# Performance work log

Measured on AMD Instinct MI355X. Metric: run time of the kernel, lower is better.

Reference implementation:

```python
import jax, jax.numpy as jnp
import numpy as np

B, S, D, V = 64, 16, 2048, 128000


def setup_inputs() -> dict:
    key = jax.random.key(0)
    k1, k2, k3, k4, k5 = jax.random.split(key, 5)
    embedding = jax.random.normal(k1, (V, D), dtype=jnp.float32) * 0.02
    hidden_states = jax.random.normal(k2, (B, S, D), dtype=jnp.float32)
    output_positions = jnp.array([S - 1], dtype=jnp.int32)  # sample from last position
    temperatures = jax.random.uniform(k3, (B,), dtype=jnp.float32, minval=0.5, maxval=1.5)
    top_ps = jax.random.uniform(k4, (B,), dtype=jnp.float32, minval=0.7, maxval=1.0)
    top_ks = jax.random.randint(k5, (B,), 1, 64).astype(jnp.int32)
    return {
        "embedding": embedding,
        "hidden_states": hidden_states,
        "output_positions": output_positions,
        "temperatures": temperatures,
        "top_ps": top_ps,
        "top_ks": top_ks,
    }


def reference(embedding, hidden_states, output_positions, temperatures, top_ps, top_ks):
    # select output position: [B, S, D] -> [B, D]
    hs = jnp.take(hidden_states, output_positions, axis=1)[:, 0, :]
    # vocab logits: [B, V]
    logits = jnp.einsum("bd,vd->bv", hs, embedding)
    logits = logits / temperatures[:, None]
    probs = jax.nn.softmax(logits.astype(jnp.float32), axis=-1)
    # descending sort of probs
    order = jnp.argsort(-probs, axis=-1)                       # [B, V]
    probs_sort = jnp.take_along_axis(probs, order, axis=-1)    # [B, V] descending
    cum = jnp.cumsum(probs_sort, axis=-1)
    # top-p: zero everything whose exclusive-prefix mass exceeds top_p
    probs_sort = jnp.where((cum - probs_sort) > top_ps[:, None], 0.0, probs_sort)
    # top-k: keep only first top_k sorted entries
    ranks = jnp.arange(V, dtype=jnp.int32)[None, :]
    probs_sort = jnp.where(ranks >= top_ks[:, None], 0.0, probs_sort)
    # renormalize
    probs_sort = probs_sort / jnp.sum(probs_sort, axis=-1, keepdims=True)
    # scatter back to original vocab order via inverse permutation
    inv = jnp.argsort(order, axis=-1)
    probs_final = jnp.take_along_axis(probs_sort, inv, axis=-1)
    # multinomial sampling (one token per row); zeros -> log 0 = -inf, excluded
    skey = jax.random.key(42)
    next_token_ids = jax.random.categorical(skey, jnp.log(probs_final), axis=-1)
    return next_token_ids
```

## Files before the change

kernel.cpp:

```cpp
#include <hip/hip_runtime.h>
#include <math.h>

#define BATCH 64
#define SEQ 16
#define DIM 2048
#define VOCAB 128000

#define BM 64
#define BN 128
#define BK 32
#define NT (DIM / BK)
#define ASZ (BM * BK)
#define BSZ (BN * BK)

typedef __attribute__((ext_vector_type(8))) short bf16x8;
typedef __attribute__((ext_vector_type(4))) float f32x4;

__device__ __forceinline__ unsigned cvt_pk_bf16(float a, float b) {
  unsigned r;
  asm("v_cvt_pk_bf16_f32 %0, %1, %2" : "=v"(r) : "v"(a), "v"(b));
  return r;
}

__device__ __forceinline__ void split8(float4 x0, float4 x1, bf16x8* hi, bf16x8* lo) {
  float f[8] = {x0.x, x0.y, x0.z, x0.w, x1.x, x1.y, x1.z, x1.w};
  union { unsigned u[4]; bf16x8 v; } H, L;
#pragma unroll
  for (int w = 0; w < 4; ++w) {
    float a = f[2 * w], b = f[2 * w + 1];
    unsigned hp = cvt_pk_bf16(a, b);
    float ha = __uint_as_float(hp << 16);
    float hb = __uint_as_float(hp & 0xffff0000u);
    H.u[w] = hp;
    L.u[w] = cvt_pk_bf16(a - ha, b - hb);
  }
  *hi = H.v;
  *lo = L.v;
}

__device__ __forceinline__ void gload_lds16(const float* src, float* lds_dst) {
  __builtin_amdgcn_global_load_lds(
      (const __attribute__((address_space(1))) void*)src,
      (__attribute__((address_space(3))) void*)lds_dst, 16, 0, 0);
}

__global__ __launch_bounds__(256, 3) void logits_kernel(
    const float* __restrict__ emb,
    const float* __restrict__ hs,
    const int* __restrict__ pos,
    const float* __restrict__ temps,
    float* __restrict__ logits) {
  __shared__ float ldsA[2 * ASZ];
  __shared__ float ldsB[2 * BSZ];

  const int tid = threadIdx.x;
  const int lane = tid & 63;
  const int wid = tid >> 6;
  const int lrow = lane & 15;
  const int lkb = lane >> 4;
  const int vb = blockIdx.x * BN + wid * 32;
  const int p = pos[0];

  const int r8 = (lane >> 3) & 7;
  const int c8 = lane & 7;
  const int cswz = 4 * (c8 ^ r8);

  const float* aSrc[2];
  float* aDst[2];
#pragma unroll
  for (int q = 0; q < 2; ++q) {
    const int g = wid * 2 + q;
    const int R = g * 8 + r8;
    aSrc[q] = hs + ((size_t)R * SEQ + p) * DIM + cswz;
    aDst[q] = &ldsA[g * 8 * BK];
  }
  const float* bSrc[4];
  float* bDst[4];
#pragma unroll
  for (int q = 0; q < 4; ++q) {
    const int g = wid * 4 + q;
    const int R = g * 8 + r8;
    bSrc[q] = emb + (size_t)(blockIdx.x * BN + R) * DIM + cswz;
    bDst[q] = &ldsB[g * 8 * BK];
  }

  f32x4 acc[4][2];
#pragma unroll
  for (int i = 0; i < 4; ++i)
#pragma unroll
    for (int j = 0; j < 2; ++j) acc[i][j] = (f32x4){0.f, 0.f, 0.f, 0.f};

  const int sfr = 4 * (lrow & 7);
  const int off0 = (lkb * 8) ^ sfr;
  const int off1 = off0 ^ 4;

#pragma unroll
  for (int q = 0; q < 2; ++q) gload_lds16(aSrc[q], aDst[q]);
#pragma unroll
  for (int q = 0; q < 4; ++q) gload_lds16(bSrc[q], bDst[q]);

  int cur = 0;
  for (int t = 0; t < NT; ++t) {
    __syncthreads();

    if (t + 1 < NT) {
      const int kof = (t + 1) * BK;
      const int ao = (cur ^ 1) * ASZ;
      const int bo = (cur ^ 1) * BSZ;
#pragma unroll
      for (int q = 0; q < 2; ++q) gload_lds16(aSrc[q] + kof, aDst[q] + ao);
#pragma unroll
      for (int q = 0; q < 4; ++q) gload_lds16(bSrc[q] + kof, bDst[q] + bo);
    }

    const float* A = &ldsA[cur * ASZ];
    const float* B = &ldsB[cur * BSZ];
    bf16x8 ah[4], al[4], bh[2], bl[2];
#pragma unroll
    for (int i = 0; i < 4; ++i) {
      const float* rb = &A[(16 * i + lrow) * BK];
      split8(*(const float4*)(rb + off0), *(const float4*)(rb + off1),
             &ah[i], &al[i]);
    }
#pragma unroll
    for (int j = 0; j < 2; ++j) {
      const float* rb = &B[(wid * 32 + 16 * j + lrow) * BK];
      split8(*(const float4*)(rb + off0), *(const float4*)(rb + off1),
             &bh[j], &bl[j]);
    }
#pragma unroll
    for (int i = 0; i < 4; ++i)
#pragma unroll
      for (int j = 0; j < 2; ++j) {
        acc[i][j] = __builtin_amdgcn_mfma_f32_16x16x32_bf16(ah[i], bh[j], acc[i][j], 0, 0, 0);
        acc[i][j] = __builtin_amdgcn_mfma_f32_16x16x32_bf16(ah[i], bl[j], acc[i][j], 0, 0, 0);
        acc[i][j] = __builtin_amdgcn_mfma_f32_16x16x32_bf16(al[i], bh[j], acc[i][j], 0, 0, 0);
      }
    cur ^= 1;
  }

#pragma unroll
  for (int i = 0; i < 4; ++i)
#pragma unroll
    for (int r = 0; r < 4; ++r) {
      const int b = 16 * i + lkb * 4 + r;
      const float tt = temps[b];
#pragma unroll
      for (int j = 0; j < 2; ++j) {
        const int v = vb + 16 * j + lrow;
        logits[(size_t)b * VOCAB + v] = acc[i][j][r] / tt;
      }
    }
}

__device__ __forceinline__ void threefry2x32(unsigned k0, unsigned k1,
                                             unsigned x0, unsigned x1,
                                             unsigned* o0, unsigned* o1) {
  const unsigned k2 = k0 ^ k1 ^ 0x1BD11BDAu;
  const unsigned ks[3] = {k0, k1, k2};
  const int rotA[4] = {13, 15, 26, 6};
  const int rotB[4] = {17, 29, 16, 24};
  x0 += k0;
  x1 += k1;
#pragma unroll
  for (int i = 0; i < 5; ++i) {
    const int* rr = (i & 1) ? rotB : rotA;
#pragma unroll
    for (int q = 0; q < 4; ++q) {
      x0 += x1;
      x1 = (x1 << rr[q]) | (x1 >> (32 - rr[q]));
      x1 ^= x0;
    }
    x0 += ks[(i + 1) % 3];
    x1 += ks[(i + 2) % 3] + (unsigned)(i + 1);
  }
  *o0 = x0;
  *o1 = x1;
}

__device__ float gumbel_noise(unsigned flat) {
  unsigned o0, o1;
  threefry2x32(0u, 42u, 0u, flat, &o0, &o1);
  unsigned bits = o0 ^ o1;
  unsigned fb = (bits >> 9) | 0x3f800000u;
  float u = __uint_as_float(fb) - 1.0f;
  const float tiny = 1.17549435e-38f;
  u = fmaxf(u, tiny);
  return -logf(-logf(u));
}

#define CAP 4096
#define NL 12
#define NTH 1024
#define NWAVE 16

__device__ __forceinline__ unsigned sortkey(float x) {
  unsigned bits = __float_as_uint(x);
  return (bits & 0x80000000u) ? ~bits : (bits | 0x80000000u);
}
__device__ __forceinline__ float inv_sortkey(unsigned u) {
  unsigned bits = (u & 0x80000000u) ? (u & 0x7fffffffu) : ~u;
  return __uint_as_float(bits);
}

__global__ __launch_bounds__(NTH) void sample_kernel(
    const float* __restrict__ logits,
    const float* __restrict__ top_ps,
    const int* __restrict__ top_ks,
    const float* __restrict__ temps,
    const int* __restrict__ pos,
    int ws_ok,
    int* __restrict__ out) {
  const int b = blockIdx.x;
  const int tid = threadIdx.x;
  const int lane = tid & 63;
  const int wave = tid >> 6;
  const float* row = logits + (size_t)b * VOCAB;
  const float4* row4 = (const float4*)row;
  const int N4 = VOCAB / 4;

  __shared__ float sred[NWAVE];
  __shared__ int scnt_sh[NL];
  __shared__ float smax, sz;
  __shared__ float sdelta;
  __shared__ unsigned scnt;
  __shared__ unsigned ubuf[CAP];
  __shared__ unsigned ibuf[CAP];
  __shared__ unsigned sorted_u[64];
  __shared__ unsigned sorted_i[64];

  const float D[NL] = {0.5f, 0.75f, 1.0f, 1.25f, 1.5f, 1.75f,
                       2.0f, 2.5f, 3.0f, 4.0f, 8.0f, 1e30f};

  float lmax = -__builtin_huge_valf();
  for (int i = tid; i < N4; i += NTH) {
    float4 v = row4[i];
    lmax = fmaxf(fmaxf(lmax, v.x), fmaxf(fmaxf(v.y, v.z), v.w));
  }
#pragma unroll
  for (int s = 32; s > 0; s >>= 1) lmax = fmaxf(lmax, __shfl_xor(lmax, s, 64));
  if (lane == 0) sred[wave] = lmax;
  if (tid < NL) scnt_sh[tid] = 0;
  __syncthreads();
  if (tid == 0) {
    float m = sred[0];
#pragma unroll
    for (int w = 1; w < NWAVE; ++w) m = fmaxf(m, sred[w]);
    smax = m;
  }
  __syncthreads();
  const float maxl = smax;

  float zsum = 0.f;
  int cnt[NL];
#pragma unroll
  for (int r = 0; r < NL; ++r) cnt[r] = 0;
  for (int i = tid; i < N4; i += NTH) {
    float4 v = row4[i];
    float xs[4] = {v.x, v.y, v.z, v.w};
#pragma unroll
    for (int c = 0; c < 4; ++c) {
      float x = xs[c];
      zsum += expf(x - maxl);
      float d = maxl - x;
#pragma unroll
      for (int r = 0; r < NL; ++r) cnt[r] += (d <= D[r]) ? 1 : 0;
    }
  }
#pragma unroll
  for (int s = 32; s > 0; s >>= 1) {
    zsum += __shfl_xor(zsum, s, 64);
#pragma unroll
    for (int r = 0; r < NL; ++r) cnt[r] += __shfl_xor(cnt[r], s, 64);
  }
  if (lane == 0) {
    sred[wave] = zsum;
#pragma unroll
    for (int r = 0; r < NL; ++r) atomicAdd(&scnt_sh[r], cnt[r]);
  }
  __syncthreads();
  if (tid == 0) {
    float z = 0.f;
#pragma unroll
    for (int w = 0; w < NWAVE; ++w) z += sred[w];
    sz = z;
    float dd = 1e30f;
#pragma unroll
    for (int r = NL - 1; r >= 0; --r)
      if (scnt_sh[r] >= 64) dd = D[r];
    sdelta = dd;
    scnt = 0;
  }
  __syncthreads();
  const float Z = sz;
  const float thrv = maxl - sdelta;

  for (int i = tid; i < N4; i += NTH) {
    float4 v = row4[i];
    float xs[4] = {v.x, v.y, v.z, v.w};
#pragma unroll
    for (int c = 0; c < 4; ++c) {
      if (xs[c] >= thrv) {
        unsigned slot = atomicAdd(&scnt, 1u);
        if (slot < CAP) {
          ubuf[slot] = sortkey(xs[c]);
          ibuf[slot] = (unsigned)(i * 4 + c);
        }
      }
    }
  }
  __syncthreads();
  const int n = (int)(scnt < (unsigned)CAP ? scnt : (unsigned)CAP);

  if (tid < 64) { sorted_u[tid] = 0u; sorted_i[tid] = 0u; }
  __syncthreads();
  for (int c = tid; c < n; c += NTH) {
    unsigned u = ubuf[c], idx = ibuf[c];
    int rank = 0;
    for (int j = 0; j < n; ++j) {
      unsigned uj = ubuf[j];
      rank += (uj > u) || (uj == u && ibuf[j] < idx);
    }
    if (rank < 64) { sorted_u[rank] = u; sorted_i[rank] = idx; }
  }
  __syncthreads();

  if (tid == 0) {
    const float topp = top_ps[b];
    const int k = top_ks[b];
    const float tval = temps[b];
    float cum = 0.f;
    float best = -__builtin_huge_valf();
    int bestidx = 0;
    for (int r = 0; r < 64 && r < n; ++r) {
      float x = inv_sortkey(sorted_u[r]);
      float pr = expf(x - maxl) / Z;
      cum += pr;
      bool keep = (r < k) && !((cum - pr) > topp) && (pr > 0.f);
      if (keep) {
        float g = gumbel_noise((unsigned)b * (unsigned)VOCAB + sorted_i[r]);
        float sc = x + g;
        if (sc > best) { best = sc; bestidx = (int)sorted_i[r]; }
      }
    }
    int token = bestidx;

    unsigned kat0, kat1;
    threefry2x32(0u, 0u, 0u, 0u, &kat0, &kat1);
    bool inputs_ok = (pos[0] >= 0 && pos[0] < SEQ) &&
                     (tval > 0.45f && tval < 1.55f) &&
                     (topp > 0.65f && topp <= 1.0f) &&
                     (k >= 1 && k < 64);
    if (!inputs_ok) token = 3333333;
    else if (!ws_ok) token = 7777777;
    else if (kat0 != 0x6b200159u || kat1 != 0x99ba4efeu) token = 5555555;
    else if (scnt > (unsigned)CAP || n < 64) token = 4444444;
    out[b] = token;
  }
}

extern "C" void kernel_launch(void* const* d_in, const int* in_sizes, int n_in,
                              void* d_out, int out_size, void* d_ws, size_t ws_size,
                              hipStream_t stream) {
  const float* emb   = (const float*)d_in[0];
  const float* hs    = (const float*)d_in[1];
  const int*   pos   = (const int*)d_in[2];
  const float* temps = (const float*)d_in[3];
  const float* topps = (const float*)d_in[4];
  const int*   topks = (const int*)d_in[5];
  float* logits = (float*)d_ws;
  int* out = (int*)d_out;

  const size_t need = (size_t)BATCH * VOCAB * sizeof(float);
  const int ws_ok = (ws_size >= need) ? 1 : 0;

  hipLaunchKernelGGL(logits_kernel, dim3(VOCAB / BN), dim3(256), 0, stream,
                     emb, hs, pos, temps, logits);
  hipLaunchKernelGGL(sample_kernel, dim3(BATCH), dim3(NTH), 0, stream,
                     logits, topps, topks, temps, pos, ws_ok, out);
}
```

Baseline: 371.1 us.

## Deepen GEMM prefetch to two stages in flight with explicit vmcnt waits

Restructures the logits GEMM main loop so two K-tiles are issued ahead. Each iteration waits only until the older tile has landed (vmcnt), reads its LDS fragments into registers, then barriers and reuses that buffer for tile t+2 before doing the split and MFMA work. This is meant to hide global-to-LDS latency better than the previous single-stage prefetch with a full __syncthreads. In exchange it adds a second barrier per iteration and more registers to hold the staged fragments, and it relies on the hand-written waitcnt values being correct.

```diff
diff --git a/kernel.cpp b/kernel.cpp
--- a/kernel.cpp
+++ b/kernel.cpp
@@ -94,40 +94,56 @@
   const int off0 = (lkb * 8) ^ sfr;
   const int off1 = off0 ^ 4;
 
-#pragma unroll
-  for (int q = 0; q < 2; ++q) gload_lds16(aSrc[q], aDst[q]);
-#pragma unroll
-  for (int q = 0; q < 4; ++q) gload_lds16(bSrc[q], bDst[q]);
-
-  int cur = 0;
+#define STAGE(T, BUF)                                                        \
+  do {                                                                       \
+    const int kof_ = (T) * BK;                                               \
+    const int ao_ = (BUF) * ASZ;                                             \
+    const int bo_ = (BUF) * BSZ;                                             \
+    _Pragma("unroll")                                                        \
+    for (int q = 0; q < 2; ++q) gload_lds16(aSrc[q] + kof_, aDst[q] + ao_);  \
+    _Pragma("unroll")                                                        \
+    for (int q = 0; q < 4; ++q) gload_lds16(bSrc[q] + kof_, bDst[q] + bo_);  \
+  } while (0)
+
+  STAGE(0, 0);
+  STAGE(1, 1);
+
   for (int t = 0; t < NT; ++t) {
-    __syncthreads();
-
-    if (t + 1 < NT) {
-      const int kof = (t + 1) * BK;
-      const int ao = (cur ^ 1) * ASZ;
-      const int bo = (cur ^ 1) * BSZ;
-#pragma unroll
-      for (int q = 0; q < 2; ++q) gload_lds16(aSrc[q] + kof, aDst[q] + ao);
-#pragma unroll
-      for (int q = 0; q < 4; ++q) gload_lds16(bSrc[q] + kof, bDst[q] + bo);
-    }
+    const int cur = t & 1;
+    if (t < NT - 1) {
+      asm volatile("s_waitcnt vmcnt(6)" ::: "memory");
+    } else {
+      asm volatile("s_waitcnt vmcnt(0)" ::: "memory");
+    }
+    __builtin_amdgcn_sched_barrier(0);
+    __builtin_amdgcn_s_barrier();
 
     const float* A = &ldsA[cur * ASZ];
     const float* B = &ldsB[cur * BSZ];
+    float4 ra[4][2], rb[2][2];
+#pragma unroll
+    for (int i = 0; i < 4; ++i) {
+      const float* rbase = &A[(16 * i + lrow) * BK];
+      ra[i][0] = *(const float4*)(rbase + off0);
+      ra[i][1] = *(const float4*)(rbase + off1);
+    }
+#pragma unroll
+    for (int j = 0; j < 2; ++j) {
+      const float* rbase = &B[(wid * 32 + 16 * j + lrow) * BK];
+      rb[j][0] = *(const float4*)(rbase + off0);
+      rb[j][1] = *(const float4*)(rbase + off1);
+    }
+    asm volatile("s_waitcnt lgkmcnt(0)" ::: "memory");
+    __builtin_amdgcn_sched_barrier(0);
+    __builtin_amdgcn_s_barrier();
+
+    if (t + 2 < NT) STAGE(t + 2, cur);
+
     bf16x8 ah[4], al[4], bh[2], bl[2];
 #pragma unroll
-    for (int i = 0; i < 4; ++i) {
-      const float* rb = &A[(16 * i + lrow) * BK];
-      split8(*(const float4*)(rb + off0), *(const float4*)(rb + off1),
-             &ah[i], &al[i]);
-    }
-#pragma unroll
-    for (int j = 0; j < 2; ++j) {
-      const float* rb = &B[(wid * 32 + 16 * j + lrow) * BK];
-      split8(*(const float4*)(rb + off0), *(const float4*)(rb + off1),
-             &bh[j], &bl[j]);
-    }
+    for (int i = 0; i < 4; ++i) split8(ra[i][0], ra[i][1], &ah[i], &al[i]);
+#pragma unroll
+    for (int j = 0; j < 2; ++j) split8(rb[j][0], rb[j][1], &bh[j], &bl[j]);
 #pragma unroll
     for (int i = 0; i < 4; ++i)
 #pragma unroll
@@ -136,8 +152,8 @@
         acc[i][j] = __builtin_amdgcn_mfma_f32_16x16x32_bf16(ah[i], bl[j], acc[i][j], 0, 0, 0);
         acc[i][j] = __builtin_amdgcn_mfma_f32_16x16x32_bf16(al[i], bh[j], acc[i][j], 0, 0, 0);
       }
-    cur ^= 1;
-  }
+  }
+#undef STAGE
 
 #pragma unroll
   for (int i = 0; i < 4; ++i)
```

After: 330.3 us. 1.12x faster.
